# Optimization experiments

Measured on AMD Instinct MI355X. Metric: run time of the kernel, lower is better.

## Reference

```python
import jax, jax.numpy as jnp
import numpy as np

D_PAIR = 128
D_HIDDEN = 128
EPS = 1e-5


def layer_norm(x, w, b):
    mu = jnp.mean(x, axis=-1, keepdims=True)
    var = jnp.var(x, axis=-1, keepdims=True)
    return (x - mu) * jax.lax.rsqrt(var + EPS) * w + b


def setup_inputs() -> dict:
    key = jax.random.key(0)
    ks = jax.random.split(key, 8)
    B, N, D, H = 1, 512, D_PAIR, D_HIDDEN
    pair = jax.random.normal(ks[0], (B, N, N, D), dtype=jnp.float32)
    # torch Linear weight layout: [out_features, in_features]
    p_in_w = jax.random.normal(ks[1], (2 * H, D), dtype=jnp.float32) / np.sqrt(D)
    g_in_w = jax.random.normal(ks[2], (2 * H, D), dtype=jnp.float32) / np.sqrt(D)
    p_out_w = jax.random.normal(ks[3], (D, H), dtype=jnp.float32) / np.sqrt(H)
    g_out_w = jax.random.normal(ks[4], (D, D), dtype=jnp.float32) / np.sqrt(D)
    ln_in_w = jnp.ones((D,), jnp.float32)
    ln_in_b = jnp.zeros((D,), jnp.float32)
    ln_out_w = jnp.ones((H,), jnp.float32)
    ln_out_b = jnp.zeros((H,), jnp.float32)
    return {
        "pair": pair,
        "ln_in_w": ln_in_w, "ln_in_b": ln_in_b,
        "p_in_w": p_in_w, "g_in_w": g_in_w,
        "ln_out_w": ln_out_w, "ln_out_b": ln_out_b,
        "p_out_w": p_out_w, "g_out_w": g_out_w,
    }


def reference(pair, ln_in_w, ln_in_b, p_in_w, g_in_w, ln_out_w, ln_out_b, p_out_w, g_out_w):
    H = D_HIDDEN
    L = pair.shape[1]
    pair_norm = layer_norm(pair, ln_in_w, ln_in_b)           # [B,N,N,D]
    p = jnp.einsum('bijd,hd->bijh', pair_norm, p_in_w)       # [B,N,N,2H]
    g = jax.nn.sigmoid(jnp.einsum('bijd,hd->bijh', pair_norm, g_in_w))
    left = g[..., :H] * p[..., :H]
    right = g[..., H:] * p[..., H:]
    # outgoing direction
    out = jnp.einsum('bikd,bjkd->bijd', left, right / jnp.float32(L))
    out = layer_norm(out, ln_out_w, ln_out_b)
    out = jnp.einsum('bijh,dh->bijd', out, p_out_w)
    gate = jax.nn.sigmoid(jnp.einsum('bijd,ed->bije', pair_norm, g_out_w))
    return gate * out
```

## Files before the change

kernel.cpp:

```cpp
#include <hip/hip_runtime.h>

#define NSEQ 512
#define RTOT (NSEQ*NSEQ)
#define DM 128

typedef unsigned short ushort_t;
using short8 = __attribute__((ext_vector_type(8))) short;
using f32x4  = __attribute__((ext_vector_type(4))) float;

__device__ __forceinline__ unsigned short f2bf(float x){
  union { float f; unsigned int u; } v; v.f = x;
  unsigned int r = v.u + 0x7fffu + ((v.u >> 16) & 1u);
  return (unsigned short)(r >> 16);
}
__device__ __forceinline__ float bf2f(unsigned short u){
  union { unsigned int u; float f; } v; v.u = ((unsigned int)u) << 16;
  return v.f;
}
__device__ __forceinline__ unsigned int pack2(float a, float b){
  return (unsigned int)f2bf(a) | ((unsigned int)f2bf(b) << 16);
}
__device__ __forceinline__ float sigmoidf(float x){ return 1.0f/(1.0f + __expf(-x)); }

__global__ __launch_bounds__(256) void k0_ln_in(const float* __restrict__ pair,
                                                const float* __restrict__ w,
                                                const float* __restrict__ b,
                                                ushort_t* __restrict__ lnx){
  int wv = threadIdx.x >> 6, lane = threadIdx.x & 63;
  size_t row = (size_t)blockIdx.x * 4 + wv;
  const float2* src = (const float2*)(pair + row * DM);
  float2 v = src[lane];
  float s = v.x + v.y, s2 = v.x*v.x + v.y*v.y;
  #pragma unroll
  for (int off = 32; off; off >>= 1){ s += __shfl_xor(s, off); s2 += __shfl_xor(s2, off); }
  float mu = s * (1.f/DM);
  float rstd = rsqrtf(s2*(1.f/DM) - mu*mu + 1e-5f);
  float o0 = (v.x - mu)*rstd*w[2*lane]   + b[2*lane];
  float o1 = (v.y - mu)*rstd*w[2*lane+1] + b[2*lane+1];
  ((unsigned int*)(lnx + row * DM))[lane] = pack2(o0, o1);
}

__global__ __launch_bounds__(256) void k1_inproj(const ushort_t* __restrict__ lnx,
                                                 const float* __restrict__ p_in_w,
                                                 const float* __restrict__ g_in_w,
                                                 ushort_t* __restrict__ left,
                                                 ushort_t* __restrict__ right){
  __shared__ __align__(16) ushort_t A[64][136];
  __shared__ __align__(16) ushort_t B[128][136];
  int tid = threadIdx.x;
  int job = blockIdx.x;
  int bm  = blockIdx.y;
  int wrow0 = ((job >= 2) ? 128 : 0) + (job & 1) * 64;
  ushort_t* outp = (job >= 2) ? right : left;
  int dbase = (job & 1) * 64;
  size_t arow0 = (size_t)bm * 64;

  #pragma unroll
  for (int it = 0; it < 4; it++){
    int e = (tid + it*256) * 8; int r = e >> 7, c = e & 127;
    *(uint4*)&A[r][c] = *(const uint4*)&lnx[(arow0 + r)*DM + c];
  }
  #pragma unroll
  for (int it = 0; it < 16; it++){
    int e = (tid + it*256) * 4; int r = e >> 7, c = e & 127;
    const float* srcw = (r < 64) ? (p_in_w + (size_t)(wrow0 + r)*DM + c)
                                 : (g_in_w + (size_t)(wrow0 + r - 64)*DM + c);
    float4 wv = *(const float4*)srcw;
    uint2 pk; pk.x = pack2(wv.x, wv.y); pk.y = pack2(wv.z, wv.w);
    *(uint2*)&B[r][c] = pk;
  }
  __syncthreads();

  int w = tid >> 6, lane = tid & 63, m = lane & 15, quad = lane >> 4;
  f32x4 acc[8];
  #pragma unroll
  for (int i = 0; i < 8; i++) acc[i] = (f32x4){0.f,0.f,0.f,0.f};
  #pragma unroll
  for (int k0 = 0; k0 < 128; k0 += 32){
    short8 a = *(const short8*)&A[w*16 + m][k0 + quad*8];
    #pragma unroll
    for (int c = 0; c < 8; c++){
      short8 bf = *(const short8*)&B[c*16 + m][k0 + quad*8];
      acc[c] = __builtin_amdgcn_mfma_f32_16x16x32_bf16(a, bf, acc[c], 0, 0, 0);
    }
  }
  size_t r0 = arow0 + w*16 + quad*4;
  #pragma unroll
  for (int c = 0; c < 4; c++){
    int d = dbase + c*16 + m;
    uint2 pk;
    pk.x = pack2(sigmoidf(acc[c+4][0]) * acc[c][0], sigmoidf(acc[c+4][1]) * acc[c][1]);
    pk.y = pack2(sigmoidf(acc[c+4][2]) * acc[c][2], sigmoidf(acc[c+4][3]) * acc[c][3]);
    *(uint2*)&outp[(size_t)d * RTOT + r0] = pk;
  }
}

__global__ __launch_bounds__(256) void k2_tri(const ushort_t* __restrict__ left,
                                              const ushort_t* __restrict__ right,
                                              ushort_t* __restrict__ tri){
  __shared__ __align__(16) ushort_t As[64][72];
  __shared__ __align__(16) ushort_t Bs[64][72];
  int tid = threadIdx.x;
  int jb = blockIdx.x, ib = blockIdx.y, d = blockIdx.z;
  const ushort_t* Ap = left  + (size_t)d * RTOT;
  const ushort_t* Bp = right + (size_t)d * RTOT;
  int i0 = ib*64, j0 = jb*64;
  int w = tid >> 6, lane = tid & 63, m = lane & 15, quad = lane >> 4;
  f32x4 acc[4];
  #pragma unroll
  for (int i = 0; i < 4; i++) acc[i] = (f32x4){0.f,0.f,0.f,0.f};

  for (int kt = 0; kt < NSEQ; kt += 64){
    __syncthreads();
    #pragma unroll
    for (int it = 0; it < 2; it++){
      int e = (tid + it*256) * 8; int r = e >> 6, c = e & 63;
      *(uint4*)&As[r][c] = *(const uint4*)&Ap[(size_t)(i0 + r)*NSEQ + kt + c];
      *(uint4*)&Bs[r][c] = *(const uint4*)&Bp[(size_t)(j0 + r)*NSEQ + kt + c];
    }
    __syncthreads();
    #pragma unroll
    for (int kk = 0; kk < 64; kk += 32){
      short8 a = *(const short8*)&As[w*16 + m][kk + quad*8];
      #pragma unroll
      for (int c = 0; c < 4; c++){
        short8 bf = *(const short8*)&Bs[c*16 + m][kk + quad*8];
        acc[c] = __builtin_amdgcn_mfma_f32_16x16x32_bf16(a, bf, acc[c], 0, 0, 0);
      }
    }
  }
  const float scale = 1.f / (float)NSEQ;
  ushort_t* outp = tri + (size_t)d * RTOT;
  #pragma unroll
  for (int c = 0; c < 4; c++){
    #pragma unroll
    for (int rr = 0; rr < 4; rr++){
      int row = i0 + w*16 + quad*4 + rr;
      int col = j0 + c*16 + m;
      outp[(size_t)row * NSEQ + col] = f2bf(acc[c][rr] * scale);
    }
  }
}

__global__ __launch_bounds__(256) void k3_out(const ushort_t* __restrict__ tri,
                                              const ushort_t* __restrict__ lnx,
                                              const float* __restrict__ lnw,
                                              const float* __restrict__ lnb,
                                              const float* __restrict__ p_out_w,
                                              const float* __restrict__ g_out_w,
                                              float* __restrict__ out){
  __shared__ __align__(16) ushort_t A1[64][136];
  __shared__ __align__(16) ushort_t A2[64][136];
  __shared__ __align__(16) ushort_t Bt[64][136];
  int tid = threadIdx.x;
  size_t r0 = (size_t)blockIdx.x * 64;

  #pragma unroll
  for (int it = 0; it < 4; it++){
    int e = (tid + it*256) * 8; int r = e >> 7, c = e & 127;
    *(uint4*)&A2[r][c] = *(const uint4*)&lnx[(r0 + r)*DM + c];
  }
  {
    int dch = tid >> 1, half = tid & 1;
    const ushort_t* src = tri + (size_t)dch * RTOT + r0 + half*32;
    #pragma unroll
    for (int q = 0; q < 4; q++){
      uint4 v = *(const uint4*)(src + q*8);
      int rb = half*32 + q*8;
      A1[rb+0][dch] = (ushort_t)(v.x & 0xffff); A1[rb+1][dch] = (ushort_t)(v.x >> 16);
      A1[rb+2][dch] = (ushort_t)(v.y & 0xffff); A1[rb+3][dch] = (ushort_t)(v.y >> 16);
      A1[rb+4][dch] = (ushort_t)(v.z & 0xffff); A1[rb+5][dch] = (ushort_t)(v.z >> 16);
      A1[rb+6][dch] = (ushort_t)(v.w & 0xffff); A1[rb+7][dch] = (ushort_t)(v.w >> 16);
    }
  }
  __syncthreads();
  {
    int row = tid >> 2, part = tid & 3;
    float x[32]; float s = 0.f, s2 = 0.f;
    #pragma unroll
    for (int j = 0; j < 32; j++){ x[j] = bf2f(A1[row][part*32 + j]); s += x[j]; s2 += x[j]*x[j]; }
    s += __shfl_xor(s, 1); s2 += __shfl_xor(s2, 1);
    s += __shfl_xor(s, 2); s2 += __shfl_xor(s2, 2);
    float mu = s * (1.f/DM);
    float rstd = rsqrtf(s2*(1.f/DM) - mu*mu + 1e-5f);
    #pragma unroll
    for (int j = 0; j < 32; j++){
      int cc = part*32 + j;
      A1[row][cc] = f2bf((x[j] - mu)*rstd*lnw[cc] + lnb[cc]);
    }
  }
  __syncthreads();

  int w = tid >> 6, lane = tid & 63, m = lane & 15, quad = lane >> 4;
  #pragma unroll
  for (int ch = 0; ch < 2; ch++){
    f32x4 accp[4], accg[4];
    #pragma unroll
    for (int i = 0; i < 4; i++){ accp[i] = (f32x4){0.f,0.f,0.f,0.f}; accg[i] = (f32x4){0.f,0.f,0.f,0.f}; }

    #pragma unroll
    for (int it = 0; it < 8; it++){
      int e = (tid + it*256) * 4; int r = e >> 7, c = e & 127;
      float4 wv = *(const float4*)&p_out_w[(size_t)(ch*64 + r)*DM + c];
      uint2 pk; pk.x = pack2(wv.x, wv.y); pk.y = pack2(wv.z, wv.w);
      *(uint2*)&Bt[r][c] = pk;
    }
    __syncthreads();
    #pragma unroll
    for (int k0 = 0; k0 < 128; k0 += 32){
      short8 a = *(const short8*)&A1[w*16 + m][k0 + quad*8];
      #pragma unroll
      for (int c = 0; c < 4; c++){
        short8 bf = *(const short8*)&Bt[c*16 + m][k0 + quad*8];
        accp[c] = __builtin_amdgcn_mfma_f32_16x16x32_bf16(a, bf, accp[c], 0, 0, 0);
      }
    }
    __syncthreads();
    #pragma unroll
    for (int it = 0; it < 8; it++){
      int e = (tid + it*256) * 4; int r = e >> 7, c = e & 127;
      float4 wv = *(const float4*)&g_out_w[(size_t)(ch*64 + r)*DM + c];
      uint2 pk; pk.x = pack2(wv.x, wv.y); pk.y = pack2(wv.z, wv.w);
      *(uint2*)&Bt[r][c] = pk;
    }
    __syncthreads();
    #pragma unroll
    for (int k0 = 0; k0 < 128; k0 += 32){
      short8 a = *(const short8*)&A2[w*16 + m][k0 + quad*8];
      #pragma unroll
      for (int c = 0; c < 4; c++){
        short8 bf = *(const short8*)&Bt[c*16 + m][k0 + quad*8];
        accg[c] = __builtin_amdgcn_mfma_f32_16x16x32_bf16(a, bf, accg[c], 0, 0, 0);
      }
    }
    #pragma unroll
    for (int c = 0; c < 4; c++){
      int dcol = ch*64 + c*16 + m;
      #pragma unroll
      for (int rr = 0; rr < 4; rr++){
        size_t row = r0 + w*16 + quad*4 + rr;
        out[row * DM + dcol] = sigmoidf(accg[c][rr]) * accp[c][rr];
      }
    }
    __syncthreads();
  }
}

extern "C" void kernel_launch(void* const* d_in, const int* in_sizes, int n_in,
                              void* d_out, int out_size, void* d_ws, size_t ws_size,
                              hipStream_t stream){
  const float* pair     = (const float*)d_in[0];
  const float* ln_in_w  = (const float*)d_in[1];
  const float* ln_in_b  = (const float*)d_in[2];
  const float* p_in_w   = (const float*)d_in[3];
  const float* g_in_w   = (const float*)d_in[4];
  const float* ln_out_w = (const float*)d_in[5];
  const float* ln_out_b = (const float*)d_in[6];
  const float* p_out_w  = (const float*)d_in[7];
  const float* g_out_w  = (const float*)d_in[8];
  float* out = (float*)d_out;

  const size_t plane = (size_t)RTOT * DM;
  ushort_t* lnx   = (ushort_t*)d_ws;
  ushort_t* left  = lnx   + plane;
  ushort_t* right = left  + plane;
  ushort_t* tri   = right + plane;

  k0_ln_in <<<dim3(RTOT/4),      dim3(256), 0, stream>>>(pair, ln_in_w, ln_in_b, lnx);
  k1_inproj<<<dim3(4, RTOT/64),  dim3(256), 0, stream>>>(lnx, p_in_w, g_in_w, left, right);
  k2_tri   <<<dim3(8, 8, 128),   dim3(256), 0, stream>>>(left, right, tri);
  k3_out   <<<dim3(RTOT/64),     dim3(256), 0, stream>>>(tri, lnx, ln_out_w, ln_out_b,
                                                         p_out_w, g_out_w, out);
}
```

Baseline: 522.7 us.

## Pre-convert weights to bf16 and enlarge triangle-multiply tiles to 128x128

Adds a small prep kernel that converts the in/out projection weights to bf16 once, so the projection kernels load bf16 weights directly instead of converting fp32 in every block. The triangle kernel now uses one block per channel and row strip, computing 128x128 output tiles with 16 accumulators per wave. This raises MFMA-to-load reuse but launches only 512 blocks, each looping over four column tiles. The LayerNorm weights in the output kernel are also staged in shared memory. The prep buffers live in workspace regions that later kernels overwrite, which depends on the launch order being kept.

```diff
diff --git a/kernel.cpp b/kernel.cpp
--- a/kernel.cpp
+++ b/kernel.cpp
@@ -21,6 +21,20 @@
   return (unsigned int)f2bf(a) | ((unsigned int)f2bf(b) << 16);
 }
 __device__ __forceinline__ float sigmoidf(float x){ return 1.0f/(1.0f + __expf(-x)); }
+
+__global__ __launch_bounds__(256) void k_prep(const float* __restrict__ a,
+                                              const float* __restrict__ b,
+                                              ushort_t* __restrict__ da,
+                                              ushort_t* __restrict__ db,
+                                              int na4, int nb4){
+  int idx = blockIdx.x*256 + threadIdx.x;
+  const float* src; ushort_t* dst; int i;
+  if (idx < na4){ src = a; dst = da; i = idx; }
+  else { i = idx - na4; if (i >= nb4) return; src = b; dst = db; }
+  float4 v = *(const float4*)(src + (size_t)i*4);
+  uint2 pk; pk.x = pack2(v.x, v.y); pk.y = pack2(v.z, v.w);
+  *(uint2*)(dst + (size_t)i*4) = pk;
+}
 
 __global__ __launch_bounds__(256) void k0_ln_in(const float* __restrict__ pair,
                                                 const float* __restrict__ w,
@@ -41,8 +55,8 @@
 }
 
 __global__ __launch_bounds__(256) void k1_inproj(const ushort_t* __restrict__ lnx,
-                                                 const float* __restrict__ p_in_w,
-                                                 const float* __restrict__ g_in_w,
+                                                 const ushort_t* __restrict__ pw_bf,
+                                                 const ushort_t* __restrict__ gw_bf,
                                                  ushort_t* __restrict__ left,
                                                  ushort_t* __restrict__ right){
   __shared__ __align__(16) ushort_t A[64][136];
@@ -61,13 +75,11 @@
     *(uint4*)&A[r][c] = *(const uint4*)&lnx[(arow0 + r)*DM + c];
   }
   #pragma unroll
-  for (int it = 0; it < 16; it++){
-    int e = (tid + it*256) * 4; int r = e >> 7, c = e & 127;
-    const float* srcw = (r < 64) ? (p_in_w + (size_t)(wrow0 + r)*DM + c)
-                                 : (g_in_w + (size_t)(wrow0 + r - 64)*DM + c);
-    float4 wv = *(const float4*)srcw;
-    uint2 pk; pk.x = pack2(wv.x, wv.y); pk.y = pack2(wv.z, wv.w);
-    *(uint2*)&B[r][c] = pk;
+  for (int it = 0; it < 8; it++){
+    int e = (tid + it*256) * 8; int r = e >> 7, c = e & 127;
+    const ushort_t* srcw = (r < 64) ? &pw_bf[(size_t)(wrow0 + r)*DM + c]
+                                    : &gw_bf[(size_t)(wrow0 + r - 64)*DM + c];
+    *(uint4*)&B[r][c] = *(const uint4*)srcw;
   }
   __syncthreads();
 
@@ -98,46 +110,61 @@
 __global__ __launch_bounds__(256) void k2_tri(const ushort_t* __restrict__ left,
                                               const ushort_t* __restrict__ right,
                                               ushort_t* __restrict__ tri){
-  __shared__ __align__(16) ushort_t As[64][72];
-  __shared__ __align__(16) ushort_t Bs[64][72];
+  __shared__ __align__(16) ushort_t As[128][72];
+  __shared__ __align__(16) ushort_t Bs[128][72];
   int tid = threadIdx.x;
-  int jb = blockIdx.x, ib = blockIdx.y, d = blockIdx.z;
+  int b = blockIdx.x;
+  int d = b & 127, ti = b >> 7;
   const ushort_t* Ap = left  + (size_t)d * RTOT;
   const ushort_t* Bp = right + (size_t)d * RTOT;
-  int i0 = ib*64, j0 = jb*64;
+  ushort_t* Cp = tri + (size_t)d * RTOT;
+  int i0 = ti * 128;
   int w = tid >> 6, lane = tid & 63, m = lane & 15, quad = lane >> 4;
-  f32x4 acc[4];
-  #pragma unroll
-  for (int i = 0; i < 4; i++) acc[i] = (f32x4){0.f,0.f,0.f,0.f};
-
-  for (int kt = 0; kt < NSEQ; kt += 64){
-    __syncthreads();
-    #pragma unroll
-    for (int it = 0; it < 2; it++){
-      int e = (tid + it*256) * 8; int r = e >> 6, c = e & 63;
-      *(uint4*)&As[r][c] = *(const uint4*)&Ap[(size_t)(i0 + r)*NSEQ + kt + c];
-      *(uint4*)&Bs[r][c] = *(const uint4*)&Bp[(size_t)(j0 + r)*NSEQ + kt + c];
-    }
-    __syncthreads();
-    #pragma unroll
-    for (int kk = 0; kk < 64; kk += 32){
-      short8 a = *(const short8*)&As[w*16 + m][kk + quad*8];
+  int wr = w & 1, wc = w >> 1;
+
+  for (int tj = 0; tj < 4; tj++){
+    int j0 = tj * 128;
+    f32x4 acc[16];
+    #pragma unroll
+    for (int x = 0; x < 16; x++) acc[x] = (f32x4){0.f,0.f,0.f,0.f};
+
+    for (int kt = 0; kt < NSEQ; kt += 64){
+      __syncthreads();
+      #pragma unroll
+      for (int it = 0; it < 4; it++){
+        int e = (tid + it*256) * 8; int r = e >> 6, c = e & 63;
+        *(uint4*)&As[r][c] = *(const uint4*)&Ap[(size_t)(i0 + r)*NSEQ + kt + c];
+        *(uint4*)&Bs[r][c] = *(const uint4*)&Bp[(size_t)(j0 + r)*NSEQ + kt + c];
+      }
+      __syncthreads();
+      #pragma unroll
+      for (int kk = 0; kk < 64; kk += 32){
+        short8 a[4], bb[4];
+        #pragma unroll
+        for (int t = 0; t < 4; t++) a[t]  = *(const short8*)&As[wr*64 + t*16 + m][kk + quad*8];
+        #pragma unroll
+        for (int c = 0; c < 4; c++) bb[c] = *(const short8*)&Bs[wc*64 + c*16 + m][kk + quad*8];
+        #pragma unroll
+        for (int t = 0; t < 4; t++){
+          #pragma unroll
+          for (int c = 0; c < 4; c++){
+            acc[t*4+c] = __builtin_amdgcn_mfma_f32_16x16x32_bf16(a[t], bb[c], acc[t*4+c], 0, 0, 0);
+          }
+        }
+      }
+    }
+    const float s = 1.f / (float)NSEQ;
+    #pragma unroll
+    for (int t = 0; t < 4; t++){
       #pragma unroll
       for (int c = 0; c < 4; c++){
-        short8 bf = *(const short8*)&Bs[c*16 + m][kk + quad*8];
-        acc[c] = __builtin_amdgcn_mfma_f32_16x16x32_bf16(a, bf, acc[c], 0, 0, 0);
-      }
-    }
-  }
-  const float scale = 1.f / (float)NSEQ;
-  ushort_t* outp = tri + (size_t)d * RTOT;
-  #pragma unroll
-  for (int c = 0; c < 4; c++){
-    #pragma unroll
-    for (int rr = 0; rr < 4; rr++){
-      int row = i0 + w*16 + quad*4 + rr;
-      int col = j0 + c*16 + m;
-      outp[(size_t)row * NSEQ + col] = f2bf(acc[c][rr] * scale);
+        int col = j0 + wc*64 + c*16 + m;
+        #pragma unroll
+        for (int rr = 0; rr < 4; rr++){
+          int row = i0 + wr*64 + t*16 + quad*4 + rr;
+          Cp[(size_t)row * NSEQ + col] = f2bf(acc[t*4+c][rr] * s);
+        }
+      }
     }
   }
 }
@@ -146,15 +173,17 @@
                                               const ushort_t* __restrict__ lnx,
                                               const float* __restrict__ lnw,
                                               const float* __restrict__ lnb,
-                                              const float* __restrict__ p_out_w,
-                                              const float* __restrict__ g_out_w,
+                                              const ushort_t* __restrict__ pow_bf,
+                                              const ushort_t* __restrict__ gow_bf,
                                               float* __restrict__ out){
   __shared__ __align__(16) ushort_t A1[64][136];
   __shared__ __align__(16) ushort_t A2[64][136];
   __shared__ __align__(16) ushort_t Bt[64][136];
+  __shared__ float lw[128], lb[128];
   int tid = threadIdx.x;
   size_t r0 = (size_t)blockIdx.x * 64;
 
+  if (tid < 128){ lw[tid] = lnw[tid]; lb[tid] = lnb[tid]; }
   #pragma unroll
   for (int it = 0; it < 4; it++){
     int e = (tid + it*256) * 8; int r = e >> 7, c = e & 127;
@@ -186,7 +215,7 @@
     #pragma unroll
     for (int j = 0; j < 32; j++){
       int cc = part*32 + j;
-      A1[row][cc] = f2bf((x[j] - mu)*rstd*lnw[cc] + lnb[cc]);
+      A1[row][cc] = f2bf((x[j] - mu)*rstd*lw[cc] + lb[cc]);
     }
   }
   __syncthreads();
@@ -199,11 +228,9 @@
     for (int i = 0; i < 4; i++){ accp[i] = (f32x4){0.f,0.f,0.f,0.f}; accg[i] = (f32x4){0.f,0.f,0.f,0.f}; }
 
     #pragma unroll
-    for (int it = 0; it < 8; it++){
-      int e = (tid + it*256) * 4; int r = e >> 7, c = e & 127;
-      float4 wv = *(const float4*)&p_out_w[(size_t)(ch*64 + r)*DM + c];
-      uint2 pk; pk.x = pack2(wv.x, wv.y); pk.y = pack2(wv.z, wv.w);
-      *(uint2*)&Bt[r][c] = pk;
+    for (int it = 0; it < 4; it++){
+      int e = (tid + it*256) * 8; int r = e >> 7, c = e & 127;
+      *(uint4*)&Bt[r][c] = *(const uint4*)&pow_bf[(size_t)(ch*64 + r)*DM + c];
     }
     __syncthreads();
     #pragma unroll
@@ -217,11 +244,9 @@
     }
     __syncthreads();
     #pragma unroll
-    for (int it = 0; it < 8; it++){
-      int e = (tid + it*256) * 4; int r = e >> 7, c = e & 127;
-      float4 wv = *(const float4*)&g_out_w[(size_t)(ch*64 + r)*DM + c];
-      uint2 pk; pk.x = pack2(wv.x, wv.y); pk.y = pack2(wv.z, wv.w);
-      *(uint2*)&Bt[r][c] = pk;
+    for (int it = 0; it < 4; it++){
+      int e = (tid + it*256) * 8; int r = e >> 7, c = e & 127;
+      *(uint4*)&Bt[r][c] = *(const uint4*)&gow_bf[(size_t)(ch*64 + r)*DM + c];
     }
     __syncthreads();
     #pragma unroll
@@ -266,9 +291,16 @@
   ushort_t* right = left  + plane;
   ushort_t* tri   = right + plane;
 
+  ushort_t* pw_bf  = tri;
+  ushort_t* gw_bf  = tri + 32768;
+  ushort_t* pow_bf = left;
+  ushort_t* gow_bf = left + 16384;
+
+  k_prep   <<<dim3(64),          dim3(256), 0, stream>>>(p_in_w, g_in_w, pw_bf, gw_bf, 8192, 8192);
   k0_ln_in <<<dim3(RTOT/4),      dim3(256), 0, stream>>>(pair, ln_in_w, ln_in_b, lnx);
-  k1_inproj<<<dim3(4, RTOT/64),  dim3(256), 0, stream>>>(lnx, p_in_w, g_in_w, left, right);
-  k2_tri   <<<dim3(8, 8, 128),   dim3(256), 0, stream>>>(left, right, tri);
+  k1_inproj<<<dim3(4, RTOT/64),  dim3(256), 0, stream>>>(lnx, pw_bf, gw_bf, left, right);
+  k2_tri   <<<dim3(512),         dim3(256), 0, stream>>>(left, right, tri);
+  k_prep   <<<dim3(32),          dim3(256), 0, stream>>>(p_out_w, g_out_w, pow_bf, gow_bf, 4096, 4096);
   k3_out   <<<dim3(RTOT/64),     dim3(256), 0, stream>>>(tri, lnx, ln_out_w, ln_out_b,
-                                                         p_out_w, g_out_w, out);
-}
+                                                         pow_bf, gow_bf, out);
+}
```

Measured after the change: 462.4 us. 11.5% less time.
